# Kernel tuning notes

Hardware: AMD Instinct MI355X
Metric: run time of the kernel (lower is better)

The kernel has to match this reference:

```python
import jax, jax.numpy as jnp
import numpy as np

N, E, C_IN = 100000, 800000, 128


def setup_inputs() -> dict:
    key = jax.random.key(0)
    ks = jax.random.split(key, 16)
    x = jax.random.normal(ks[0], (N, C_IN), dtype=jnp.float32)
    edge_index = jax.random.randint(ks[1], (2, E), 0, N, dtype=jnp.int64)

    def glorot(k, shape):
        lim = float(np.sqrt(6.0 / (shape[0] + shape[1])))
        return jax.random.uniform(k, shape, jnp.float32, -lim, lim)

    # channels = [128, 128, 256, 256, 256, 112]; layers 0,3 are l_GCN, layers 1,2,4 are l_SAGE
    params = dict(
        alpha=0.1 * jax.random.normal(ks[2], (5,), jnp.float32),  # ReZero alphas (init'd !=0 to exercise path)
        W0=glorot(ks[3], (128, 128)), b0=jnp.zeros((128,), jnp.float32),
        W1=glorot(ks[4], (128, 256)), R1=glorot(ks[5], (128, 256)), b1=jnp.zeros((256,), jnp.float32),
        W2=glorot(ks[6], (256, 256)), R2=glorot(ks[7], (256, 256)), b2=jnp.zeros((256,), jnp.float32),
        W3=glorot(ks[8], (256, 256)), b3=jnp.zeros((256,), jnp.float32),
        W4=glorot(ks[9], (256, 112)), R4=glorot(ks[10], (256, 112)), b4=jnp.zeros((112,), jnp.float32),
    )
    return dict(x=x, edge_index=edge_index, **params)


def reference(x, edge_index, alpha, W0, b0, W1, R1, b1, W2, R2, b2, W3, b3, W4, R4, b4):
    n = x.shape[0]
    row, col = edge_index[0], edge_index[1]
    ones = jnp.ones((row.shape[0],), x.dtype)
    deg = jax.ops.segment_sum(ones, row, num_segments=n)        # out-degree per node
    dinv = jnp.where(deg > 0, jax.lax.rsqrt(jnp.maximum(deg, 1e-12)), 0.0)
    cnt = jnp.maximum(deg, 1.0)[:, None]                        # mean-aggregation denominator

    def gcn_agg(h):  # D^-1/2 A D^-1/2 @ h
        m = h[col] * dinv[col][:, None]                          # [E, C] gather + scale
        return jax.ops.segment_sum(m, row, num_segments=n) * dinv[:, None]

    def mean_agg(h):  # SparseTensor.matmul(h, reduce='mean')
        return jax.ops.segment_sum(h[col], row, num_segments=n) / cnt

    # layer 0: l_GCN, re_list, rezero=1 -> residual from y[0]; dropout = identity (eval)
    t0 = gcn_agg(x) @ W0 + b0
    h = x + alpha[0] * t0
    # layer 1: l_SAGE + relu
    h = jax.nn.relu(mean_agg(h) @ W1 + h @ R1 + b1)
    # layer 2: l_SAGE + relu
    h = jax.nn.relu(mean_agg(h) @ W2 + h @ R2 + b2)
    # layer 3: l_GCN, re_list, rezero=1 -> residual from y[3] (current h)
    t3 = gcn_agg(h) @ W3 + b3
    h = h + alpha[3] * t3
    # layer 4: l_SAGE, no relu, no residual
    h = mean_agg(h) @ W4 + h @ R4 + b4
    return h
```

## Files before the change

kernel.cpp:

```cpp
#include <hip/hip_runtime.h>


typedef __attribute__((ext_vector_type(8))) short bf16x8;
typedef __attribute__((ext_vector_type(4))) float f32x4;

__device__ __forceinline__ float bf2f(unsigned short u) {
    union { unsigned int i; float f; } v; v.i = ((unsigned int)u) << 16; return v.f;
}
__device__ __forceinline__ unsigned short f2bf(float f) {
    union { float f; unsigned int i; } v; v.f = f;
    unsigned int r = (v.i + 0x7fffu + ((v.i >> 16) & 1u)) >> 16;
    return (unsigned short)r;
}


__global__ __launch_bounds__(256) void zero_int_kernel(int* __restrict__ p, int n)
{
    int i = blockIdx.x * 256 + threadIdx.x;
    if (i < n) p[i] = 0;
}

__global__ __launch_bounds__(256) void count_deg_kernel(
    const int* __restrict__ row, int* __restrict__ deg, int E)
{
    int e = blockIdx.x * 256 + threadIdx.x;
    if (e < E) atomicAdd(&deg[row[e]], 1);
}

__global__ __launch_bounds__(1024) void scan_p1_kernel(
    const int* __restrict__ deg, int* __restrict__ rp,
    int* __restrict__ bsum, int n)
{
    __shared__ int wsum[16];
    int t = threadIdx.x, lane = t & 63, w = t >> 6;
    int base = blockIdx.x * 2048;
    int carry = 0;
    #pragma unroll
    for (int half = 0; half < 2; ++half) {
        int i = base + half * 1024 + t;
        int xv = (i < n) ? deg[i] : 0;
        int s = xv;
        #pragma unroll
        for (int off = 1; off < 64; off <<= 1) {
            int v = __shfl_up(s, off, 64);
            if (lane >= off) s += v;
        }
        if (lane == 63) wsum[w] = s;
        __syncthreads();
        if (w == 0 && lane < 16) {
            int ws = wsum[lane];
            #pragma unroll
            for (int off = 1; off < 16; off <<= 1) {
                int v = __shfl_up(ws, off, 64);
                if (lane >= off) ws += v;
            }
            wsum[lane] = ws;
        }
        __syncthreads();
        int wo = (w == 0) ? 0 : wsum[w - 1];
        if (i < n) rp[i + 1] = carry + wo + s;
        carry += wsum[15];
        if (half == 0) __syncthreads();
    }
    if (t == 0) bsum[blockIdx.x] = carry;
}

__global__ __launch_bounds__(64) void scan_p2_kernel(int* __restrict__ bsum, int B)
{
    int lane = threadIdx.x;
    int v = (lane < B) ? bsum[lane] : 0;
    int s = v;
    #pragma unroll
    for (int off = 1; off < 64; off <<= 1) {
        int u = __shfl_up(s, off, 64);
        if (lane >= off) s += u;
    }
    if (lane < B) bsum[lane] = s - v;
}

__global__ __launch_bounds__(1024) void scan_p3_kernel(
    const int* __restrict__ deg, int* __restrict__ rp,
    int* __restrict__ cursor, const int* __restrict__ bsum,
    float* __restrict__ dinv, float* __restrict__ cinv, int n)
{
    int boff = bsum[blockIdx.x];
    int base = blockIdx.x * 2048;
    #pragma unroll
    for (int half = 0; half < 2; ++half) {
        int i = base + half * 1024 + threadIdx.x;
        if (i < n) {
            int d = deg[i];
            int incl = rp[i + 1] + boff;
            rp[i + 1] = incl;
            cursor[i] = incl - d;
            float df = (float)d;
            dinv[i] = (d > 0) ? rsqrtf(df) : 0.0f;
            cinv[i] = 1.0f / fmaxf(df, 1.0f);
        }
    }
    if (blockIdx.x == 0 && threadIdx.x == 0) rp[0] = 0;
}

__global__ __launch_bounds__(256) void fill_csr_kernel(
    const int* __restrict__ row, const int* __restrict__ col,
    int* __restrict__ cursor, int* __restrict__ colS, int E)
{
    int e = blockIdx.x * 256 + threadIdx.x;
    if (e < E) {
        int p = atomicAdd(&cursor[row[e]], 1);
        colS[p] = col[e];
    }
}


__global__ __launch_bounds__(256) void f32_to_bf16_kernel(
    const float* __restrict__ src, unsigned short* __restrict__ dst, int n4)
{
    int i = blockIdx.x * 256 + threadIdx.x;
    if (i >= n4) return;
    float4 v = ((const float4*)src)[i];
    ushort4 o;
    o.x = f2bf(v.x); o.y = f2bf(v.y); o.z = f2bf(v.z); o.w = f2bf(v.w);
    ((ushort4*)dst)[i] = o;
}

__global__ __launch_bounds__(256) void prep_w_kernel(
    const float* __restrict__ S1, int K1,
    const float* __restrict__ S2, int K2,
    int Nout, int Npad, unsigned short* __restrict__ dst)
{
    int Ktot = K1 + K2;
    int idx = blockIdx.x * 256 + threadIdx.x;
    if (idx >= Npad * Ktot) return;
    int n = idx / Ktot, k = idx - n * Ktot;
    float v = 0.0f;
    if (n < Nout)
        v = (k < K1) ? S1[(size_t)k * Nout + n] : S2[(size_t)(k - K1) * Nout + n];
    dst[idx] = f2bf(v);
}


__device__ __forceinline__ void acc8(float* acc, uint4 u, float s) {
    unsigned int xs[4] = {u.x, u.y, u.z, u.w};
    #pragma unroll
    for (int p = 0; p < 4; ++p) {
        union { unsigned int i; float f; } lo, hi;
        lo.i = xs[p] << 16;
        hi.i = xs[p] & 0xffff0000u;
        acc[2 * p]     += s * lo.f;
        acc[2 * p + 1] += s * hi.f;
    }
}

template <int C, bool HAS_ES>
__global__ __launch_bounds__(256) void agg_bf16_kernel(
    const unsigned short* __restrict__ h, int ldh,
    const int* __restrict__ rp, const int* __restrict__ cols,
    const float* __restrict__ escale, const float* __restrict__ nscale,
    unsigned short* __restrict__ out, int ldo, int n)
{
    constexpr int LPE = (C == 256) ? 32 : 16;
    constexpr int EPG = 64 / LPE;
    constexpr int UNR = 4;
    int node = blockIdx.x * 4 + (threadIdx.x >> 6);
    if (node >= n) return;
    int lane = threadIdx.x & 63;
    int grp = lane / LPE, sub = lane % LPE;
    const unsigned short* hc = h + sub * 8;

    int s = rp[node], e = rp[node + 1];
    float acc[8];
    #pragma unroll
    for (int k = 0; k < 8; ++k) acc[k] = 0.0f;

    for (int i = s; i < e; i += UNR * EPG) {
        int cc[UNR]; float sc[UNR]; uint4 uu[UNR];
        #pragma unroll
        for (int u = 0; u < UNR; ++u) {
            int ii = i + u * EPG + grp;
            bool valid = ii < e;
            int c = valid ? cols[ii] : 0;
            cc[u] = c;
            sc[u] = valid ? (HAS_ES ? escale[c] : 1.0f) : 0.0f;
        }
        #pragma unroll
        for (int u = 0; u < UNR; ++u)
            uu[u] = *(const uint4*)(hc + (size_t)cc[u] * ldh);
        #pragma unroll
        for (int u = 0; u < UNR; ++u)
            acc8(acc, uu[u], sc[u]);
    }

    #pragma unroll
    for (int k = 0; k < 8; ++k) {
        if (EPG == 4) acc[k] += __shfl_xor(acc[k], 16, 64);
        acc[k] += __shfl_xor(acc[k], 32, 64);
    }

    if (grp == 0) {
        float ns = nscale[node];
        uint4 o;
        unsigned int* op = (unsigned int*)&o;
        #pragma unroll
        for (int p = 0; p < 4; ++p) {
            unsigned short a = f2bf(acc[2 * p] * ns);
            unsigned short b = f2bf(acc[2 * p + 1] * ns);
            op[p] = (unsigned int)a | ((unsigned int)b << 16);
        }
        *(uint4*)(out + (size_t)node * ldo + sub * 8) = o;
    }
}


__device__ __forceinline__ void g2l16(const unsigned short* g, unsigned short* l) {
    __builtin_amdgcn_global_load_lds(
        (const __attribute__((address_space(1))) unsigned int*)g,
        (__attribute__((address_space(3))) unsigned int*)l, 16, 0, 0);
}

template <int BN, int EPI, bool RES_BF16, bool WF32, bool WB16>
__global__ __launch_bounds__(2 * BN) void mfma_gemm_kernel(
    const unsigned short* __restrict__ A1, int K1, int lda1,
    const unsigned short* __restrict__ A2, int K2, int lda2,
    const unsigned short* __restrict__ Bt,
    const float* __restrict__ bias,
    const void* __restrict__ res, int ldres,
    const float* __restrict__ alpha_ptr, int alpha_idx,
    float* __restrict__ outf, unsigned short* __restrict__ outb, int ldo,
    int M, int Nout)
{
    constexpr int WAVES = BN / 32;
    constexpr int AI = 256 / BN;
    __shared__ unsigned short As[2][128 * 32];
    __shared__ unsigned short Bs[2][BN * 32];
    int t = threadIdx.x;
    int m0 = blockIdx.x * 128, n0 = blockIdx.y * BN;
    int Ktot = K1 + K2;
    int w = t >> 6, lane = t & 63;
    int wm = w & 1, wn = w >> 1;
    int q = lane >> 4, l16 = lane & 15;

    int koff = (((lane & 3) ^ ((lane >> 2) & 3)) * 8);
    int rsub = lane >> 2;

    f32x4 acc[4][4];
    #pragma unroll
    for (int i = 0; i < 4; ++i)
        #pragma unroll
        for (int j = 0; j < 4; ++j)
            #pragma unroll
            for (int r = 0; r < 4; ++r) acc[i][j][r] = 0.0f;

    const int KC = Ktot >> 5;

    auto issue = [&](int kc, int p) {
        int k0 = kc * 32;
        const unsigned short* Ap; int lda, kk;
        if (k0 < K1) { Ap = A1; lda = lda1; kk = k0; }
        else         { Ap = A2; lda = lda2; kk = k0 - K1; }
        #pragma unroll
        for (int a = 0; a < AI; ++a) {
            int rb = a * 16 * WAVES + w * 16;
            int gm = m0 + rb + rsub; if (gm >= M) gm = M - 1;
            g2l16(Ap + (size_t)gm * lda + kk + koff, &As[p][rb * 32]);
        }
        #pragma unroll
        for (int b = 0; b < 2; ++b) {
            int rb = b * 16 * WAVES + w * 16;
            int gn = n0 + rb + rsub;
            g2l16(Bt + (size_t)gn * Ktot + k0 + koff, &Bs[p][rb * 32]);
        }
    };

    const int cq = (q ^ (l16 & 3)) * 8;
    const int rbA = (wm * 64 + l16) * 32 + cq;
    const int rbB = (wn * 64 + l16) * 32 + cq;

    issue(0, 0);
    if (KC > 1) issue(1, 1);

    for (int kc = 0; kc < KC; ++kc) {
        int p = kc & 1;
        int rem = KC - 1 - kc;
        if (rem >= 1) {
            if constexpr (AI == 2) asm volatile("s_waitcnt vmcnt(4)" ::: "memory");
            else                   asm volatile("s_waitcnt vmcnt(3)" ::: "memory");
        } else {
            asm volatile("s_waitcnt vmcnt(0)" ::: "memory");
        }
        __builtin_amdgcn_s_barrier();
        asm volatile("" ::: "memory");

        bf16x8 af[4], bfr[4];
        #pragma unroll
        for (int i = 0; i < 4; ++i)
            af[i] = *(const bf16x8*)&As[p][rbA + i * 16 * 32];
        #pragma unroll
        for (int j = 0; j < 4; ++j)
            bfr[j] = *(const bf16x8*)&Bs[p][rbB + j * 16 * 32];

        asm volatile("s_waitcnt lgkmcnt(0)" ::: "memory");
        __builtin_amdgcn_s_barrier();
        asm volatile("" ::: "memory");
        if (kc + 2 < KC) issue(kc + 2, p);

        __builtin_amdgcn_s_setprio(1);
        #pragma unroll
        for (int i = 0; i < 4; ++i)
            #pragma unroll
            for (int j = 0; j < 4; ++j)
                acc[i][j] = __builtin_amdgcn_mfma_f32_16x16x32_bf16(
                    af[i], bfr[j], acc[i][j], 0, 0, 0);
        __builtin_amdgcn_s_setprio(0);
    }

    float alpha = 0.0f;
    if (EPI == 2) alpha = alpha_ptr[alpha_idx];
    #pragma unroll
    for (int i = 0; i < 4; ++i) {
        #pragma unroll
        for (int j = 0; j < 4; ++j) {
            int n = n0 + wn * 64 + j * 16 + l16;
            if (n >= Nout) continue;
            float bv = bias[n];
            #pragma unroll
            for (int r = 0; r < 4; ++r) {
                int m = m0 + wm * 64 + i * 16 + q * 4 + r;
                if (m >= M) continue;
                float v = acc[i][j][r] + bv;
                if (EPI == 1) v = fmaxf(v, 0.0f);
                if (EPI == 2) {
                    float r0 = RES_BF16
                        ? bf2f(((const unsigned short*)res)[(size_t)m * ldres + n])
                        : ((const float*)res)[(size_t)m * ldres + n];
                    v = r0 + alpha * v;
                }
                if (WF32) outf[(size_t)m * ldo + n] = v;
                if (WB16) outb[(size_t)m * ldo + n] = f2bf(v);
            }
        }
    }
}


extern "C" void kernel_launch(void* const* d_in, const int* in_sizes, int n_in,
                              void* d_out, int out_size, void* d_ws, size_t ws_size,
                              hipStream_t stream)
{
    const float* x      = (const float*)d_in[0];
    const int*   ei     = (const int*)d_in[1];
    const float* alpha  = (const float*)d_in[2];
    const float* W0     = (const float*)d_in[3];
    const float* b0     = (const float*)d_in[4];
    const float* W1     = (const float*)d_in[5];
    const float* R1     = (const float*)d_in[6];
    const float* b1     = (const float*)d_in[7];
    const float* W2     = (const float*)d_in[8];
    const float* R2     = (const float*)d_in[9];
    const float* b2     = (const float*)d_in[10];
    const float* W3     = (const float*)d_in[11];
    const float* b3     = (const float*)d_in[12];
    const float* W4     = (const float*)d_in[13];
    const float* R4     = (const float*)d_in[14];
    const float* b4     = (const float*)d_in[15];

    const int N = in_sizes[0] / 128;
    const int E = in_sizes[1] / 2;
    const int* row = ei;
    const int* col = ei + E;

    size_t off = 0;
    auto alloc = [&](size_t bytes) -> void* {
        void* p = (char*)d_ws + off;
        off += (bytes + 255) & ~(size_t)255;
        return p;
    };
    int*   deg    = (int*)alloc((size_t)N * 4);
    int*   rp     = (int*)alloc((size_t)(N + 1) * 4);
    int*   cursor = (int*)alloc((size_t)N * 4);
    int*   colS   = (int*)alloc((size_t)E * 4);
    int*   bsum   = (int*)alloc((size_t)64 * 4);
    float* dinv   = (float*)alloc((size_t)N * 4);
    float* cinv   = (float*)alloc((size_t)N * 4);
    unsigned short* Wt0 = (unsigned short*)alloc((size_t)128 * 128 * 2);
    unsigned short* Wt1 = (unsigned short*)alloc((size_t)256 * 256 * 2);
    unsigned short* Wt2 = (unsigned short*)alloc((size_t)256 * 512 * 2);
    unsigned short* Wt3 = (unsigned short*)alloc((size_t)256 * 256 * 2);
    unsigned short* Wt4 = (unsigned short*)alloc((size_t)128 * 512 * 2);
    unsigned short* Xb  = (unsigned short*)alloc((size_t)N * 128 * 2);
    unsigned short* Gb  = (unsigned short*)alloc((size_t)N * 256 * 2);
    unsigned short* Pb  = (unsigned short*)alloc((size_t)N * 256 * 2);
    unsigned short* Ab  = (unsigned short*)alloc((size_t)N * 256 * 2);
    unsigned short* Hb  = Xb;
    (void)ws_size;

    const int SB = (N + 2047) / 2048;
    zero_int_kernel<<<(N + 255) / 256, 256, 0, stream>>>(deg, N);
    count_deg_kernel<<<(E + 255) / 256, 256, 0, stream>>>(row, deg, E);
    scan_p1_kernel<<<SB, 1024, 0, stream>>>(deg, rp, bsum, N);
    scan_p2_kernel<<<1, 64, 0, stream>>>(bsum, SB);
    scan_p3_kernel<<<SB, 1024, 0, stream>>>(deg, rp, cursor, bsum, dinv, cinv, N);
    fill_csr_kernel<<<(E + 255) / 256, 256, 0, stream>>>(row, col, cursor, colS, E);

    f32_to_bf16_kernel<<<(N * 32 + 255) / 256, 256, 0, stream>>>(x, Xb, N * 32);
    prep_w_kernel<<<(128 * 128 + 255) / 256, 256, 0, stream>>>(W0, 128, nullptr, 0, 128, 128, Wt0);
    prep_w_kernel<<<(256 * 256 + 255) / 256, 256, 0, stream>>>(W1, 128, R1, 128, 256, 256, Wt1);
    prep_w_kernel<<<(256 * 512 + 255) / 256, 256, 0, stream>>>(W2, 256, R2, 256, 256, 256, Wt2);
    prep_w_kernel<<<(256 * 256 + 255) / 256, 256, 0, stream>>>(W3, 256, nullptr, 0, 256, 256, Wt3);
    prep_w_kernel<<<(128 * 512 + 255) / 256, 256, 0, stream>>>(W4, 256, R4, 256, 112, 128, Wt4);

    dim3 aggGrid((N + 3) / 4);
    dim3 g1((N + 127) / 128, 1);

    agg_bf16_kernel<128, true><<<aggGrid, 256, 0, stream>>>(Xb, 128, rp, colS, dinv, dinv, Ab, 128, N);
    mfma_gemm_kernel<128, 2, false, false, true><<<g1, 256, 0, stream>>>(
        Ab, 128, 128, nullptr, 0, 0, Wt0, b0, x, 128, alpha, 0,
        nullptr, Hb, 128, N, 128);

    agg_bf16_kernel<128, false><<<aggGrid, 256, 0, stream>>>(Hb, 128, rp, colS, nullptr, cinv, Ab, 128, N);
    mfma_gemm_kernel<256, 1, false, false, true><<<g1, 512, 0, stream>>>(
        Ab, 128, 128, Hb, 128, 128, Wt1, b1, nullptr, 0, nullptr, 0,
        nullptr, Gb, 256, N, 256);

    agg_bf16_kernel<256, false><<<aggGrid, 256, 0, stream>>>(Gb, 256, rp, colS, nullptr, cinv, Ab, 256, N);
    mfma_gemm_kernel<256, 1, false, false, true><<<g1, 512, 0, stream>>>(
        Ab, 256, 256, Gb, 256, 256, Wt2, b2, nullptr, 0, nullptr, 0,
        nullptr, Pb, 256, N, 256);

    agg_bf16_kernel<256, true><<<aggGrid, 256, 0, stream>>>(Pb, 256, rp, colS, dinv, dinv, Ab, 256, N);
    mfma_gemm_kernel<256, 2, true, false, true><<<g1, 512, 0, stream>>>(
        Ab, 256, 256, nullptr, 0, 0, Wt3, b3, Pb, 256, alpha, 3,
        nullptr, Gb, 256, N, 256);

    agg_bf16_kernel<256, false><<<aggGrid, 256, 0, stream>>>(Gb, 256, rp, colS, nullptr, cinv, Ab, 256, N);
    mfma_gemm_kernel<128, 0, false, true, false><<<g1, 256, 0, stream>>>(
        Ab, 256, 256, Gb, 256, 256, Wt4, b4, nullptr, 0, nullptr, 0,
        (float*)d_out, nullptr, 112, N, 112);
}
```

Baseline: 727.3 us.

## Switch activations to fp16 with packed half-precision aggregation and vectorized GEMM epilogue

After: 690.9 us. -5.0%, faster.

```diff
diff --git a/kernel.cpp b/kernel.cpp
--- a/kernel.cpp
+++ b/kernel.cpp
@@ -1,16 +1,15 @@
 #include <hip/hip_runtime.h>
 
 
-typedef __attribute__((ext_vector_type(8))) short bf16x8;
+typedef _Float16 __attribute__((ext_vector_type(8))) f16x8;
+typedef _Float16 __attribute__((ext_vector_type(2))) f16x2;
 typedef __attribute__((ext_vector_type(4))) float f32x4;
 
-__device__ __forceinline__ float bf2f(unsigned short u) {
-    union { unsigned int i; float f; } v; v.i = ((unsigned int)u) << 16; return v.f;
-}
-__device__ __forceinline__ unsigned short f2bf(float f) {
-    union { float f; unsigned int i; } v; v.f = f;
-    unsigned int r = (v.i + 0x7fffu + ((v.i >> 16) & 1u)) >> 16;
-    return (unsigned short)r;
+__device__ __forceinline__ unsigned short f2h(float f) {
+    union { _Float16 h; unsigned short u; } v; v.h = (_Float16)f; return v.u;
+}
+__device__ __forceinline__ float h2f(unsigned short u) {
+    union { unsigned short u; _Float16 h; } v; v.u = u; return (float)v.h;
 }
 
 
@@ -113,14 +112,14 @@
 }
 
 
-__global__ __launch_bounds__(256) void f32_to_bf16_kernel(
+__global__ __launch_bounds__(256) void f32_to_f16_kernel(
     const float* __restrict__ src, unsigned short* __restrict__ dst, int n4)
 {
     int i = blockIdx.x * 256 + threadIdx.x;
     if (i >= n4) return;
     float4 v = ((const float4*)src)[i];
     ushort4 o;
-    o.x = f2bf(v.x); o.y = f2bf(v.y); o.z = f2bf(v.z); o.w = f2bf(v.w);
+    o.x = f2h(v.x); o.y = f2h(v.y); o.z = f2h(v.z); o.w = f2h(v.w);
     ((ushort4*)dst)[i] = o;
 }
 
@@ -136,24 +135,12 @@
     float v = 0.0f;
     if (n < Nout)
         v = (k < K1) ? S1[(size_t)k * Nout + n] : S2[(size_t)(k - K1) * Nout + n];
-    dst[idx] = f2bf(v);
-}
-
-
-__device__ __forceinline__ void acc8(float* acc, uint4 u, float s) {
-    unsigned int xs[4] = {u.x, u.y, u.z, u.w};
-    #pragma unroll
-    for (int p = 0; p < 4; ++p) {
-        union { unsigned int i; float f; } lo, hi;
-        lo.i = xs[p] << 16;
-        hi.i = xs[p] & 0xffff0000u;
-        acc[2 * p]     += s * lo.f;
-        acc[2 * p + 1] += s * hi.f;
-    }
-}
+    dst[idx] = f2h(v);
+}
+
 
 template <int C, bool HAS_ES>
-__global__ __launch_bounds__(256) void agg_bf16_kernel(
+__global__ __launch_bounds__(256) void agg_f16_kernel(
     const unsigned short* __restrict__ h, int ldh,
     const int* __restrict__ rp, const int* __restrict__ cols,
     const float* __restrict__ escale, const float* __restrict__ nscale,
@@ -169,45 +156,53 @@
     const unsigned short* hc = h + sub * 8;
 
     int s = rp[node], e = rp[node + 1];
-    float acc[8];
-    #pragma unroll
-    for (int k = 0; k < 8; ++k) acc[k] = 0.0f;
+    const _Float16 hz = (_Float16)0.0f;
+    f16x2 zz = { hz, hz };
+    f16x2 acc2[4];
+    #pragma unroll
+    for (int k = 0; k < 4; ++k) acc2[k] = zz;
 
     for (int i = s; i < e; i += UNR * EPG) {
-        int cc[UNR]; float sc[UNR]; uint4 uu[UNR];
+        int cc[UNR]; f16x2 ssv[UNR]; uint4 uu[UNR];
         #pragma unroll
         for (int u = 0; u < UNR; ++u) {
             int ii = i + u * EPG + grp;
             bool valid = ii < e;
             int c = valid ? cols[ii] : 0;
             cc[u] = c;
-            sc[u] = valid ? (HAS_ES ? escale[c] : 1.0f) : 0.0f;
+            float sc = valid ? (HAS_ES ? escale[c] : 1.0f) : 0.0f;
+            _Float16 sh = (_Float16)sc;
+            f16x2 sv = { sh, sh };
+            ssv[u] = sv;
         }
         #pragma unroll
         for (int u = 0; u < UNR; ++u)
             uu[u] = *(const uint4*)(hc + (size_t)cc[u] * ldh);
         #pragma unroll
-        for (int u = 0; u < UNR; ++u)
-            acc8(acc, uu[u], sc[u]);
-    }
-
-    #pragma unroll
-    for (int k = 0; k < 8; ++k) {
-        if (EPG == 4) acc[k] += __shfl_xor(acc[k], 16, 64);
-        acc[k] += __shfl_xor(acc[k], 32, 64);
+        for (int u = 0; u < UNR; ++u) {
+            union { uint4 q; f16x2 hh[4]; } cv; cv.q = uu[u];
+            #pragma unroll
+            for (int p = 0; p < 4; ++p)
+                acc2[p] += cv.hh[p] * ssv[u];
+        }
+    }
+
+    #pragma unroll
+    for (int k = 0; k < 4; ++k) {
+        union { f16x2 h2; float f; } a, b;
+        a.h2 = acc2[k];
+        if (EPG == 4) { b.f = __shfl_xor(a.f, 16, 64); a.h2 = a.h2 + b.h2; }
+        b.f = __shfl_xor(a.f, 32, 64); a.h2 = a.h2 + b.h2;
+        acc2[k] = a.h2;
     }
 
     if (grp == 0) {
-        float ns = nscale[node];
-        uint4 o;
-        unsigned int* op = (unsigned int*)&o;
-        #pragma unroll
-        for (int p = 0; p < 4; ++p) {
-            unsigned short a = f2bf(acc[2 * p] * ns);
-            unsigned short b = f2bf(acc[2 * p + 1] * ns);
-            op[p] = (unsigned int)a | ((unsigned int)b << 16);
-        }
-        *(uint4*)(out + (size_t)node * ldo + sub * 8) = o;
+        _Float16 nh = (_Float16)nscale[node];
+        f16x2 nn = { nh, nh };
+        union { uint4 q; f16x2 hh[4]; } o;
+        #pragma unroll
+        for (int p = 0; p < 4; ++p) o.hh[p] = acc2[p] * nn;
+        *(uint4*)(out + (size_t)node * ldo + sub * 8) = o.q;
     }
 }
 
@@ -218,7 +213,7 @@
         (__attribute__((address_space(3))) unsigned int*)l, 16, 0, 0);
 }
 
-template <int BN, int EPI, bool RES_BF16, bool WF32, bool WB16>
+template <int BN, int EPI, bool RES_F16, bool WF32, bool WB16>
 __global__ __launch_bounds__(2 * BN) void mfma_gemm_kernel(
     const unsigned short* __restrict__ A1, int K1, int lda1,
     const unsigned short* __restrict__ A2, int K2, int lda2,
@@ -291,13 +286,13 @@
         __builtin_amdgcn_s_barrier();
         asm volatile("" ::: "memory");
 
-        bf16x8 af[4], bfr[4];
+        f16x8 af[4], bfr[4];
         #pragma unroll
         for (int i = 0; i < 4; ++i)
-            af[i] = *(const bf16x8*)&As[p][rbA + i * 16 * 32];
+            af[i] = *(const f16x8*)&As[p][rbA + i * 16 * 32];
         #pragma unroll
         for (int j = 0; j < 4; ++j)
-            bfr[j] = *(const bf16x8*)&Bs[p][rbB + j * 16 * 32];
+            bfr[j] = *(const f16x8*)&Bs[p][rbB + j * 16 * 32];
 
         asm volatile("s_waitcnt lgkmcnt(0)" ::: "memory");
         __builtin_amdgcn_s_barrier();
@@ -309,8 +304,8 @@
         for (int i = 0; i < 4; ++i)
             #pragma unroll
             for (int j = 0; j < 4; ++j)
-                acc[i][j] = __builtin_amdgcn_mfma_f32_16x16x32_bf16(
-                    af[i], bfr[j], acc[i][j], 0, 0, 0);
+                acc[i][j] = __builtin_amdgcn_mfma_f32_16x16x32_f16(
+                    bfr[j], af[i], acc[i][j], 0, 0, 0);
         __builtin_amdgcn_s_setprio(0);
     }
 
@@ -318,25 +313,44 @@
     if (EPI == 2) alpha = alpha_ptr[alpha_idx];
     #pragma unroll
     for (int i = 0; i < 4; ++i) {
+        int m = m0 + wm * 64 + i * 16 + l16;
+        if (m >= M) continue;
         #pragma unroll
         for (int j = 0; j < 4; ++j) {
-            int n = n0 + wn * 64 + j * 16 + l16;
-            if (n >= Nout) continue;
-            float bv = bias[n];
-            #pragma unroll
-            for (int r = 0; r < 4; ++r) {
-                int m = m0 + wm * 64 + i * 16 + q * 4 + r;
-                if (m >= M) continue;
-                float v = acc[i][j][r] + bv;
-                if (EPI == 1) v = fmaxf(v, 0.0f);
-                if (EPI == 2) {
-                    float r0 = RES_BF16
-                        ? bf2f(((const unsigned short*)res)[(size_t)m * ldres + n])
-                        : ((const float*)res)[(size_t)m * ldres + n];
-                    v = r0 + alpha * v;
+            int nb = n0 + wn * 64 + j * 16 + q * 4;
+            if (nb >= Nout) continue;
+            float4 bv = *(const float4*)&bias[nb];
+            float v0 = acc[i][j][0] + bv.x;
+            float v1 = acc[i][j][1] + bv.y;
+            float v2 = acc[i][j][2] + bv.z;
+            float v3 = acc[i][j][3] + bv.w;
+            if (EPI == 1) {
+                v0 = fmaxf(v0, 0.0f); v1 = fmaxf(v1, 0.0f);
+                v2 = fmaxf(v2, 0.0f); v3 = fmaxf(v3, 0.0f);
+            }
+            if (EPI == 2) {
+                if (RES_F16) {
+                    ushort4 rr = *(const ushort4*)
+                        ((const unsigned short*)res + (size_t)m * ldres + nb);
+                    v0 = h2f(rr.x) + alpha * v0;
+                    v1 = h2f(rr.y) + alpha * v1;
+                    v2 = h2f(rr.z) + alpha * v2;
+                    v3 = h2f(rr.w) + alpha * v3;
+                } else {
+                    float4 rr = *(const float4*)
+                        ((const float*)res + (size_t)m * ldres + nb);
+                    v0 = rr.x + alpha * v0;
+                    v1 = rr.y + alpha * v1;
+                    v2 = rr.z + alpha * v2;
+                    v3 = rr.w + alpha * v3;
                 }
-                if (WF32) outf[(size_t)m * ldo + n] = v;
-                if (WB16) outb[(size_t)m * ldo + n] = f2bf(v);
+            }
+            if (WF32) {
+                *(float4*)&outf[(size_t)m * ldo + nb] = make_float4(v0, v1, v2, v3);
+            }
+            if (WB16) {
+                *(ushort4*)&outb[(size_t)m * ldo + nb] =
+                    make_ushort4(f2h(v0), f2h(v1), f2h(v2), f2h(v3));
             }
         }
     }
@@ -402,7 +416,7 @@
     scan_p3_kernel<<<SB, 1024, 0, stream>>>(deg, rp, cursor, bsum, dinv, cinv, N);
     fill_csr_kernel<<<(E + 255) / 256, 256, 0, stream>>>(row, col, cursor, colS, E);
 
-    f32_to_bf16_kernel<<<(N * 32 + 255) / 256, 256, 0, stream>>>(x, Xb, N * 32);
+    f32_to_f16_kernel<<<(N * 32 + 255) / 256, 256, 0, stream>>>(x, Xb, N * 32);
     prep_w_kernel<<<(128 * 128 + 255) / 256, 256, 0, stream>>>(W0, 128, nullptr, 0, 128, 128, Wt0);
     prep_w_kernel<<<(256 * 256 + 255) / 256, 256, 0, stream>>>(W1, 128, R1, 128, 256, 256, Wt1);
     prep_w_kernel<<<(256 * 512 + 255) / 256, 256, 0, stream>>>(W2, 256, R2, 256, 256, 256, Wt2);
@@ -412,27 +426,27 @@
     dim3 aggGrid((N + 3) / 4);
     dim3 g1((N + 127) / 128, 1);
 
-    agg_bf16_kernel<128, true><<<aggGrid, 256, 0, stream>>>(Xb, 128, rp, colS, dinv, dinv, Ab, 128, N);
+    agg_f16_kernel<128, true><<<aggGrid, 256, 0, stream>>>(Xb, 128, rp, colS, dinv, dinv, Ab, 128, N);
     mfma_gemm_kernel<128, 2, false, false, true><<<g1, 256, 0, stream>>>(
         Ab, 128, 128, nullptr, 0, 0, Wt0, b0, x, 128, alpha, 0,
         nullptr, Hb, 128, N, 128);
 
-    agg_bf16_kernel<128, false><<<aggGrid, 256, 0, stream>>>(Hb, 128, rp, colS, nullptr, cinv, Ab, 128, N);
+    agg_f16_kernel<128, false><<<aggGrid, 256, 0, stream>>>(Hb, 128, rp, colS, nullptr, cinv, Ab, 128, N);
     mfma_gemm_kernel<256, 1, false, false, true><<<g1, 512, 0, stream>>>(
         Ab, 128, 128, Hb, 128, 128, Wt1, b1, nullptr, 0, nullptr, 0,
         nullptr, Gb, 256, N, 256);
 
-    agg_bf16_kernel<256, false><<<aggGrid, 256, 0, stream>>>(Gb, 256, rp, colS, nullptr, cinv, Ab, 256, N);
+    agg_f16_kernel<256, false><<<aggGrid, 256, 0, stream>>>(Gb, 256, rp, colS, nullptr, cinv, Ab, 256, N);
     mfma_gemm_kernel<256, 1, false, false, true><<<g1, 512, 0, stream>>>(
         Ab, 256, 256, Gb, 256, 256, Wt2, b2, nullptr, 0, nullptr, 0,
         nullptr, Pb, 256, N, 256);
 
-    agg_bf16_kernel<256, true><<<aggGrid, 256, 0, stream>>>(Pb, 256, rp, colS, dinv, dinv, Ab, 256, N);
+    agg_f16_kernel<256, true><<<aggGrid, 256, 0, stream>>>(Pb, 256, rp, colS, dinv, dinv, Ab, 256, N);
     mfma_gemm_kernel<256, 2, true, false, true><<<g1, 512, 0, stream>>>(
         Ab, 256, 256, nullptr, 0, 0, Wt3, b3, Pb, 256, alpha, 3,
         nullptr, Gb, 256, N, 256);
 
-    agg_bf16_kernel<256, false><<<aggGrid, 256, 0, stream>>>(Gb, 256, rp, colS, nullptr, cinv, Ab, 256, N);
+    agg_f16_kernel<256, false><<<aggGrid, 256, 0, stream>>>(Gb, 256, rp, colS, nullptr, cinv, Ab, 256, N);
     mfma_gemm_kernel<128, 0, false, true, false><<<g1, 256, 0, stream>>>(
         Ab, 256, 256, Gb, 256, 256, Wt4, b4, nullptr, 0, nullptr, 0,
         (float*)d_out, nullptr, 112, N, 112);
```
